# Performance work log

Measured on AMD Instinct MI355X. Metric: run time of the kernel, lower is better.

Reference implementation:

```python
import jax, jax.numpy as jnp
import numpy as np
from itertools import product

B, C, HH, WW, DD, N = 2, 32, 96, 96, 96, 30000


def setup_inputs() -> dict:
    key = jax.random.key(0)
    k1, k2, k3 = jax.random.split(key, 3)
    voxel_features = jax.random.normal(k1, (B, C, HH, WW, DD), dtype=jnp.float32)
    # vertices in normalized [-1, 1] grid_sample coordinates (x, y, z)
    vertices = jax.random.uniform(k2, (B, N, 3), dtype=jnp.float32, minval=-1.0, maxval=1.0)
    fan_in = C * 27
    conv_w = jax.random.normal(k3, (C, C, 1, 27), dtype=jnp.float32) * np.sqrt(2.0 / fan_in)
    conv_b = jnp.zeros((C,), dtype=jnp.float32)
    return {
        "voxel_features": voxel_features,
        "vertices": vertices,
        "conv_w": conv_w,
        "conv_b": conv_b,
        "img_H": HH,
        "img_W": WW,
        "img_D": DD,
    }


def _trilinear_sample(voxel_features, grid):
    """grid_sample(mode='bilinear', padding_mode='border', align_corners=True).
    voxel_features: (B,C,H,W,D); grid: (B,N,K,3) with (x,y,z) in [-1,1],
    x -> D axis, y -> W axis, z -> H axis. Returns (B,C,N,K)."""
    b, c, h, w, d = voxel_features.shape
    x, y, z = grid[..., 0], grid[..., 1], grid[..., 2]
    ix = jnp.clip((x + 1.0) * 0.5 * (d - 1), 0.0, d - 1)
    iy = jnp.clip((y + 1.0) * 0.5 * (w - 1), 0.0, w - 1)
    iz = jnp.clip((z + 1.0) * 0.5 * (h - 1), 0.0, h - 1)
    x0 = jnp.floor(ix).astype(jnp.int32); x1 = jnp.minimum(x0 + 1, d - 1)
    y0 = jnp.floor(iy).astype(jnp.int32); y1 = jnp.minimum(y0 + 1, w - 1)
    z0 = jnp.floor(iz).astype(jnp.int32); z1 = jnp.minimum(z0 + 1, h - 1)
    fx = ix - x0; fy = iy - y0; fz = iz - z0
    vf = voxel_features.reshape(b, c, h * w * d)
    n, k = grid.shape[1], grid.shape[2]

    def gather(zi, yi, xi):
        lin = (zi * w + yi) * d + xi  # (B,N,K)
        g = jnp.take_along_axis(vf, lin.reshape(b, 1, n * k), axis=2)
        return g.reshape(b, c, n, k)

    def wgt(wz, wy, wx):
        return (wz * wy * wx)[:, None]  # (B,1,N,K)

    out = (
        gather(z0, y0, x0) * wgt(1 - fz, 1 - fy, 1 - fx)
        + gather(z0, y0, x1) * wgt(1 - fz, 1 - fy, fx)
        + gather(z0, y1, x0) * wgt(1 - fz, fy, 1 - fx)
        + gather(z0, y1, x1) * wgt(1 - fz, fy, fx)
        + gather(z1, y0, x0) * wgt(fz, 1 - fy, 1 - fx)
        + gather(z1, y0, x1) * wgt(fz, 1 - fy, fx)
        + gather(z1, y1, x0) * wgt(fz, fy, 1 - fx)
        + gather(z1, y1, x1) * wgt(fz, fy, fx)
    )
    return out


def reference(voxel_features, vertices, conv_w, conv_b, img_H, img_W, img_D):
    # 27 neighbor offsets in normalized coords, scaled per (x,y,z) component
    offs = jnp.asarray(list(product((-1, 0, 1), repeat=3)), dtype=jnp.float32)  # (27,3)
    scale = jnp.array(
        [2.0 / (img_D - 1), 2.0 / (img_W - 1), 2.0 / (img_H - 1)], dtype=jnp.float32
    )
    shift = offs * scale  # (27,3)
    grid = vertices[:, :, None, :] + shift[None, None]  # (B,N,27,3)
    feats = _trilinear_sample(voxel_features, grid)  # (B,C,N,27)
    # Conv2d(C,C,(1,27)): weighted reduction over (C_in, 27) -> (B,N,C_out)
    out = jnp.einsum("bink,oik->bno", feats, conv_w[:, :, 0, :]) + conv_b
    return out
```

## Files before the change

kernel.cpp:

```cpp
#include <hip/hip_runtime.h>
#include <stdint.h>

#define HWD 884736ull
#define NV 30000
#define AST 1032

typedef __attribute__((ext_vector_type(8))) __bf16 bf16x8;
typedef __attribute__((ext_vector_type(4))) float f32x4;
typedef __attribute__((ext_vector_type(2))) float f32x2;
typedef __attribute__((ext_vector_type(4))) unsigned int uint4v;

__device__ __forceinline__ unsigned short f2bf(float f) {
    union { float f; unsigned int u; } v; v.f = f;
    unsigned int u = v.u;
    return (unsigned short)((u + 0x7FFFu + ((u >> 16) & 1u)) >> 16);
}

__device__ __forceinline__ unsigned short bfc(float f) {
    __bf16 h = (__bf16)f;
    unsigned short u;
    __builtin_memcpy(&u, &h, 2);
    return u;
}

__device__ __forceinline__ unsigned int pkbf(float lo, float hi) {
    __bf16 a = (__bf16)lo, b = (__bf16)hi;
    unsigned short ua, ub;
    __builtin_memcpy(&ua, &a, 2);
    __builtin_memcpy(&ub, &b, 2);
    return (unsigned int)ua | ((unsigned int)ub << 16);
}

__device__ __forceinline__ f32x2 up2(unsigned int u) {
    union { unsigned int u; float f; } lo, hi;
    lo.u = u << 16;
    hi.u = u & 0xFFFF0000u;
    f32x2 r; r.x = lo.f; r.y = hi.f;
    return r;
}

__device__ __forceinline__ void axis_setup(float coord, float sc, int& wstart, float w[3][4]) {
    int i0[3], i1[3];
    float fr[3];
#pragma unroll
    for (int a = 0; a < 3; ++a) {
        float g = coord + (float)(a - 1) * sc;
        float ix = (g + 1.0f) * 0.5f * 95.0f;
        ix = fminf(fmaxf(ix, 0.0f), 95.0f);
        float fl = floorf(ix);
        int x0 = (int)fl;
        i0[a] = x0;
        i1[a] = min(x0 + 1, 95);
        fr[a] = ix - fl;
    }
    int ws = min(max(i0[1] - 1, 0), 92);
    wstart = ws;
#pragma unroll
    for (int a = 0; a < 3; ++a) {
        int d0 = min(max(i0[a] - ws, 0), 3);
        int d1 = min(max(i1[a] - ws, 0), 3);
        float f1 = fr[a], f0 = 1.0f - f1;
#pragma unroll
        for (int j = 0; j < 4; ++j)
            w[a][j] = (d0 == j ? f0 : 0.0f) + (d1 == j ? f1 : 0.0f);
    }
}

__global__ __launch_bounds__(256) void prep_kernel(const float* __restrict__ cw,
                                                   unsigned short* __restrict__ Wp) {
    int gid = blockIdx.x * 256 + threadIdx.x;
    int j = gid & 7;
    int l = (gid >> 3) & 63;
    int t = (gid >> 9) & 1;
    int s = gid >> 10;
    int kk = ((l >> 4) & 3) * 8 + j;
    int o = t * 16 + (l & 15);
    float v = 0.0f;
    if (kk < 27) v = cw[(size_t)o * 864 + s * 27 + kk];
    Wp[gid] = f2bf(v);
}

__global__ __launch_bounds__(256) void transpose_kernel(const float* __restrict__ vox,
                                                        unsigned short* __restrict__ voxT) {
    __shared__ unsigned short T[192 * 40];
    int blk = blockIdx.x;
    int tid = threadIdx.x;
    int b = blk / 4608;
    int zy = blk - b * 4608;
    const float* src = vox + (size_t)b * 32 * HWD + (size_t)zy * 192;
    int c = tid >> 3;
    int xs = tid & 7;
    const float* srcc = src + (size_t)c * HWD;
#pragma unroll
    for (int i = 0; i < 6; ++i) {
        int x4 = xs + 8 * i;
        f32x4 v = *(const f32x4*)(srcc + x4 * 4);
#pragma unroll
        for (int k = 0; k < 4; ++k)
            T[(x4 * 4 + k) * 40 + c] = bfc(v[k]);
    }
    __syncthreads();
    unsigned short* dst = voxT + (size_t)blk * 6144;
#pragma unroll
    for (int i = 0; i < 3; ++i) {
        int q = i * 256 + tid;
        int x = q >> 2;
        int cg = (q & 3) * 8;
        uint4v val = *(const uint4v*)&T[x * 40 + cg];
        *(uint4v*)(dst + q * 8) = val;
    }
}

__global__ __launch_bounds__(256) void fused_kernel(const unsigned short* __restrict__ voxT,
                                                    const float* __restrict__ verts,
                                                    const unsigned short* __restrict__ Wp,
                                                    const float* __restrict__ bias,
                                                    float* __restrict__ out) {
    __shared__ unsigned short At[16 * AST];
    int tid = threadIdx.x;
    int vl = tid >> 4;
    int cp = tid & 15;
    int vg = (int)blockIdx.x * 16 + vl;

    const float* vp = verts + (size_t)vg * 3;
    float vx = vp[0], vy = vp[1], vz = vp[2];
    const float sc = 2.0f / 95.0f;
    int wsx, wsy, wsz;
    float wx[3][4], wy[3][4], wz[3][4];
    axis_setup(vx, sc, wsx, wx);
    axis_setup(vy, sc, wsy, wy);
    axis_setup(vz, sc, wsz, wz);
    int bb = (vg >= NV) ? 1 : 0;
    const unsigned short* vb = voxT + (size_t)bb * HWD * 32 + 2 * cp;

    f32x2 zz = {0.f, 0.f};
    f32x2 f[27];
#pragma unroll
    for (int k = 0; k < 27; ++k) f[k] = zz;

#pragma unroll
    for (int tz = 0; tz < 4; ++tz) {
        f32x2 ry[3][3];
#pragma unroll
        for (int bq = 0; bq < 3; ++bq)
#pragma unroll
            for (int a = 0; a < 3; ++a) ry[bq][a] = zz;
#pragma unroll
        for (int ty = 0; ty < 4; ++ty) {
            const unsigned short* row =
                vb + (((size_t)(wsz + tz) * 96 + (size_t)(wsy + ty)) * 96 + wsx) * 32;
            unsigned int u0 = *(const unsigned int*)(row);
            unsigned int u1 = *(const unsigned int*)(row + 32);
            unsigned int u2 = *(const unsigned int*)(row + 64);
            unsigned int u3 = *(const unsigned int*)(row + 96);
            f32x2 b0 = up2(u0), b1 = up2(u1), b2 = up2(u2), b3 = up2(u3);
#pragma unroll
            for (int a = 0; a < 3; ++a) {
                f32x2 r = b0 * wx[a][0] + b1 * wx[a][1] + b2 * wx[a][2] + b3 * wx[a][3];
#pragma unroll
                for (int bq = 0; bq < 3; ++bq)
                    ry[bq][a] += r * wy[bq][ty];
            }
        }
#pragma unroll
        for (int g = 0; g < 3; ++g)
#pragma unroll
            for (int bq = 0; bq < 3; ++bq)
#pragma unroll
                for (int a = 0; a < 3; ++a)
                    f[9 * a + 3 * bq + g] += wz[g][tz] * ry[bq][a];
    }

    unsigned int pk0[16], pk1[16];
#pragma unroll
    for (int i = 0; i < 16; ++i) {
        float l0 = (2 * i < 27) ? f[2 * i].x : 0.0f;
        float h0 = (2 * i + 1 < 27) ? f[2 * i + 1].x : 0.0f;
        float l1 = (2 * i < 27) ? f[2 * i].y : 0.0f;
        float h1 = (2 * i + 1 < 27) ? f[2 * i + 1].y : 0.0f;
        pk0[i] = pkbf(l0, h0);
        pk1[i] = pkbf(l1, h1);
    }
    unsigned short* abase = &At[vl * AST + cp * 64];
    int e = cp & 7;
    {
        uint4v c0 = {pk0[0], pk0[1], pk0[2], pk0[3]};
        uint4v c1 = {pk0[4], pk0[5], pk0[6], pk0[7]};
        uint4v c2 = {pk0[8], pk0[9], pk0[10], pk0[11]};
        uint4v c3 = {pk0[12], pk0[13], pk0[14], pk0[15]};
        uint4v c4 = {pk1[0], pk1[1], pk1[2], pk1[3]};
        uint4v c5 = {pk1[4], pk1[5], pk1[6], pk1[7]};
        uint4v c6 = {pk1[8], pk1[9], pk1[10], pk1[11]};
        uint4v c7 = {pk1[12], pk1[13], pk1[14], pk1[15]};
        *(uint4v*)(abase + ((0 ^ e) << 3)) = c0;
        *(uint4v*)(abase + ((1 ^ e) << 3)) = c1;
        *(uint4v*)(abase + ((2 ^ e) << 3)) = c2;
        *(uint4v*)(abase + ((3 ^ e) << 3)) = c3;
        *(uint4v*)(abase + ((4 ^ e) << 3)) = c4;
        *(uint4v*)(abase + ((5 ^ e) << 3)) = c5;
        *(uint4v*)(abase + ((6 ^ e) << 3)) = c6;
        *(uint4v*)(abase + ((7 ^ e) << 3)) = c7;
    }

    __syncthreads();

    int wv = tid >> 6;
    if (wv < 2) {
        int lane = tid & 63;
        int mrow = lane & 15, quad = lane >> 4;
        const bf16x8* wp = (const bf16x8*)Wp;
        f32x4 acc = {0.f, 0.f, 0.f, 0.f};
#pragma unroll 8
        for (int s = 0; s < 32; ++s) {
            int cpg = s >> 1;
            int kk = ((s & 1) << 2) | quad;
            bf16x8 a = *(const bf16x8*)&At[mrow * AST + cpg * 64 + ((kk ^ (cpg & 7)) << 3)];
            bf16x8 b = wp[(s * 2 + wv) * 64 + lane];
            acc = __builtin_amdgcn_mfma_f32_16x16x32_bf16(a, b, acc, 0, 0, 0);
        }
        float bs = bias[wv * 16 + mrow];
#pragma unroll
        for (int r = 0; r < 4; ++r) {
            int v = (int)blockIdx.x * 16 + quad * 4 + r;
            out[(size_t)v * 32 + wv * 16 + mrow] = acc[r] + bs;
        }
    }
}

extern "C" void kernel_launch(void* const* d_in, const int* in_sizes, int n_in,
                              void* d_out, int out_size, void* d_ws, size_t ws_size,
                              hipStream_t stream) {
    const float* vox = (const float*)d_in[0];
    const float* verts = (const float*)d_in[1];
    const float* cw = (const float*)d_in[2];
    const float* cb = (const float*)d_in[3];
    float* out = (float*)d_out;

    unsigned short* Wp = (unsigned short*)d_ws;
    unsigned short* voxT = (unsigned short*)((char*)d_ws + 65536);

    hipLaunchKernelGGL(prep_kernel, dim3(128), dim3(256), 0, stream, cw, Wp);
    hipLaunchKernelGGL(transpose_kernel, dim3(9216), dim3(256), 0, stream, vox, voxT);
    hipLaunchKernelGGL(fused_kernel, dim3(3750), dim3(256), 0, stream,
                       voxT, verts, Wp, cb, out);
}
```

Before: 386.0 us.

## Exploit sparse z-weights, emit bf16 features directly to LDS per z-group

The z-axis interpolation now uses only the two nonzero tap indices per output z-offset instead of looping over all four z rows with mostly-zero weights. Results for each z-group are written as individual bf16 halfwords straight into the swizzled LDS tile, and the padding slots are zeroed up front. This removes the 27-entry f32x2 accumulator array to cut register pressure, and adds a launch-bounds occupancy hint of 4. The cost is 6 z-row passes instead of 4, giving more (mostly L1/L2-cached) global loads, and many scalar 2-byte LDS stores replacing eight 16-byte stores.

After: 393.0 us. No clear change (+1.8%).

```diff
diff --git a/kernel.cpp b/kernel.cpp
--- a/kernel.cpp
+++ b/kernel.cpp
@@ -21,14 +21,6 @@
     unsigned short u;
     __builtin_memcpy(&u, &h, 2);
     return u;
-}
-
-__device__ __forceinline__ unsigned int pkbf(float lo, float hi) {
-    __bf16 a = (__bf16)lo, b = (__bf16)hi;
-    unsigned short ua, ub;
-    __builtin_memcpy(&ua, &a, 2);
-    __builtin_memcpy(&ub, &b, 2);
-    return (unsigned int)ua | ((unsigned int)ub << 16);
 }
 
 __device__ __forceinline__ f32x2 up2(unsigned int u) {
@@ -63,6 +55,32 @@
 #pragma unroll
         for (int j = 0; j < 4; ++j)
             w[a][j] = (d0 == j ? f0 : 0.0f) + (d1 == j ? f1 : 0.0f);
+    }
+}
+
+__device__ __forceinline__ void axis_setup_z(float coord, float sc, int& wstart,
+                                             int dz[3][2], float fzw[3][2]) {
+    int i0[3], i1[3];
+    float fr[3];
+#pragma unroll
+    for (int a = 0; a < 3; ++a) {
+        float g = coord + (float)(a - 1) * sc;
+        float ix = (g + 1.0f) * 0.5f * 95.0f;
+        ix = fminf(fmaxf(ix, 0.0f), 95.0f);
+        float fl = floorf(ix);
+        int x0 = (int)fl;
+        i0[a] = x0;
+        i1[a] = min(x0 + 1, 95);
+        fr[a] = ix - fl;
+    }
+    int ws = min(max(i0[1] - 1, 0), 92);
+    wstart = ws;
+#pragma unroll
+    for (int a = 0; a < 3; ++a) {
+        dz[a][0] = min(max(i0[a] - ws, 0), 3);
+        dz[a][1] = min(max(i1[a] - ws, 0), 3);
+        fzw[a][0] = 1.0f - fr[a];
+        fzw[a][1] = fr[a];
     }
 }
 
@@ -111,11 +129,11 @@
     }
 }
 
-__global__ __launch_bounds__(256) void fused_kernel(const unsigned short* __restrict__ voxT,
-                                                    const float* __restrict__ verts,
-                                                    const unsigned short* __restrict__ Wp,
-                                                    const float* __restrict__ bias,
-                                                    float* __restrict__ out) {
+__global__ __launch_bounds__(256, 4) void fused_kernel(const unsigned short* __restrict__ voxT,
+                                                       const float* __restrict__ verts,
+                                                       const unsigned short* __restrict__ Wp,
+                                                       const float* __restrict__ bias,
+                                                       float* __restrict__ out) {
     __shared__ unsigned short At[16 * AST];
     int tid = threadIdx.x;
     int vl = tid >> 4;
@@ -126,80 +144,75 @@
     float vx = vp[0], vy = vp[1], vz = vp[2];
     const float sc = 2.0f / 95.0f;
     int wsx, wsy, wsz;
-    float wx[3][4], wy[3][4], wz[3][4];
+    float wx[3][4], wy[3][4];
+    int dzt[3][2];
+    float fzw[3][2];
     axis_setup(vx, sc, wsx, wx);
     axis_setup(vy, sc, wsy, wy);
-    axis_setup(vz, sc, wsz, wz);
+    axis_setup_z(vz, sc, wsz, dzt, fzw);
     int bb = (vg >= NV) ? 1 : 0;
     const unsigned short* vb = voxT + (size_t)bb * HWD * 32 + 2 * cp;
 
+    int e = cp & 7;
+    unsigned short* lanebase = &At[vl * AST + cp * 64];
+    unsigned short* bptr[8];
+#pragma unroll
+    for (int kc = 0; kc < 8; ++kc) bptr[kc] = lanebase + ((kc ^ e) << 3);
+
+#pragma unroll
+    for (int chi = 0; chi < 2; ++chi) {
+        unsigned short* p = bptr[chi * 4 + 3];
+        p[3] = 0;
+        *(unsigned long long*)(p + 4) = 0ull;
+    }
+
     f32x2 zz = {0.f, 0.f};
-    f32x2 f[27];
-#pragma unroll
-    for (int k = 0; k < 27; ++k) f[k] = zz;
-
-#pragma unroll
-    for (int tz = 0; tz < 4; ++tz) {
-        f32x2 ry[3][3];
+#pragma unroll
+    for (int g = 0; g < 3; ++g) {
+        f32x2 fg[9];
+#pragma unroll
+        for (int i = 0; i < 9; ++i) fg[i] = zz;
+#pragma unroll
+        for (int t2 = 0; t2 < 2; ++t2) {
+            int tz = dzt[g][t2];
+            float wzv = fzw[g][t2];
+            f32x2 ry[3][3];
+#pragma unroll
+            for (int bq = 0; bq < 3; ++bq)
+#pragma unroll
+                for (int a = 0; a < 3; ++a) ry[bq][a] = zz;
+#pragma unroll
+            for (int ty = 0; ty < 4; ++ty) {
+                const unsigned short* row =
+                    vb + (((size_t)(wsz + tz) * 96 + (size_t)(wsy + ty)) * 96 + wsx) * 32;
+                unsigned int u0 = *(const unsigned int*)(row);
+                unsigned int u1 = *(const unsigned int*)(row + 32);
+                unsigned int u2 = *(const unsigned int*)(row + 64);
+                unsigned int u3 = *(const unsigned int*)(row + 96);
+                f32x2 b0 = up2(u0), b1 = up2(u1), b2 = up2(u2), b3 = up2(u3);
+#pragma unroll
+                for (int a = 0; a < 3; ++a) {
+                    f32x2 r = b0 * wx[a][0] + b1 * wx[a][1] + b2 * wx[a][2] + b3 * wx[a][3];
+#pragma unroll
+                    for (int bq = 0; bq < 3; ++bq)
+                        ry[bq][a] += r * wy[bq][ty];
+                }
+            }
+#pragma unroll
+            for (int bq = 0; bq < 3; ++bq)
+#pragma unroll
+                for (int a = 0; a < 3; ++a)
+                    fg[3 * bq + a] += wzv * ry[bq][a];
+        }
 #pragma unroll
         for (int bq = 0; bq < 3; ++bq)
 #pragma unroll
-            for (int a = 0; a < 3; ++a) ry[bq][a] = zz;
-#pragma unroll
-        for (int ty = 0; ty < 4; ++ty) {
-            const unsigned short* row =
-                vb + (((size_t)(wsz + tz) * 96 + (size_t)(wsy + ty)) * 96 + wsx) * 32;
-            unsigned int u0 = *(const unsigned int*)(row);
-            unsigned int u1 = *(const unsigned int*)(row + 32);
-            unsigned int u2 = *(const unsigned int*)(row + 64);
-            unsigned int u3 = *(const unsigned int*)(row + 96);
-            f32x2 b0 = up2(u0), b1 = up2(u1), b2 = up2(u2), b3 = up2(u3);
-#pragma unroll
             for (int a = 0; a < 3; ++a) {
-                f32x2 r = b0 * wx[a][0] + b1 * wx[a][1] + b2 * wx[a][2] + b3 * wx[a][3];
-#pragma unroll
-                for (int bq = 0; bq < 3; ++bq)
-                    ry[bq][a] += r * wy[bq][ty];
+                int k1 = 9 * a + 3 * bq + g;
+                f32x2 v = fg[3 * bq + a];
+                bptr[k1 >> 3][k1 & 7] = bfc(v.x);
+                bptr[4 + (k1 >> 3)][k1 & 7] = bfc(v.y);
             }
-        }
-#pragma unroll
-        for (int g = 0; g < 3; ++g)
-#pragma unroll
-            for (int bq = 0; bq < 3; ++bq)
-#pragma unroll
-                for (int a = 0; a < 3; ++a)
-                    f[9 * a + 3 * bq + g] += wz[g][tz] * ry[bq][a];
-    }
-
-    unsigned int pk0[16], pk1[16];
-#pragma unroll
-    for (int i = 0; i < 16; ++i) {
-        float l0 = (2 * i < 27) ? f[2 * i].x : 0.0f;
-        float h0 = (2 * i + 1 < 27) ? f[2 * i + 1].x : 0.0f;
-        float l1 = (2 * i < 27) ? f[2 * i].y : 0.0f;
-        float h1 = (2 * i + 1 < 27) ? f[2 * i + 1].y : 0.0f;
-        pk0[i] = pkbf(l0, h0);
-        pk1[i] = pkbf(l1, h1);
-    }
-    unsigned short* abase = &At[vl * AST + cp * 64];
-    int e = cp & 7;
-    {
-        uint4v c0 = {pk0[0], pk0[1], pk0[2], pk0[3]};
-        uint4v c1 = {pk0[4], pk0[5], pk0[6], pk0[7]};
-        uint4v c2 = {pk0[8], pk0[9], pk0[10], pk0[11]};
-        uint4v c3 = {pk0[12], pk0[13], pk0[14], pk0[15]};
-        uint4v c4 = {pk1[0], pk1[1], pk1[2], pk1[3]};
-        uint4v c5 = {pk1[4], pk1[5], pk1[6], pk1[7]};
-        uint4v c6 = {pk1[8], pk1[9], pk1[10], pk1[11]};
-        uint4v c7 = {pk1[12], pk1[13], pk1[14], pk1[15]};
-        *(uint4v*)(abase + ((0 ^ e) << 3)) = c0;
-        *(uint4v*)(abase + ((1 ^ e) << 3)) = c1;
-        *(uint4v*)(abase + ((2 ^ e) << 3)) = c2;
-        *(uint4v*)(abase + ((3 ^ e) << 3)) = c3;
-        *(uint4v*)(abase + ((4 ^ e) << 3)) = c4;
-        *(uint4v*)(abase + ((5 ^ e) << 3)) = c5;
-        *(uint4v*)(abase + ((6 ^ e) << 3)) = c6;
-        *(uint4v*)(abase + ((7 ^ e) << 3)) = c7;
     }
 
     __syncthreads();
```

## Bin vertices spatially and remap blocks per XCD for gather locality

Applied to the files above, without the earlier changes.

Adds a counting-sort pipeline (zero, count, scan, scatter) that groups vertices into 8^3-voxel spatial bins per batch, producing a permutation. The fused kernel processes vertices in permuted order and remaps block indices so consecutive bins land on the same XCD, aiming to raise L2 hit rates for the random trilinear gathers. It adds four small kernel launches and an indirect write of outputs, and the scatter order is nondeterministic within a bin.

Result: slower. 414.6 us (+7.4%).

```diff
diff --git a/kernel.cpp b/kernel.cpp
--- a/kernel.cpp
+++ b/kernel.cpp
@@ -4,6 +4,7 @@
 #define HWD 884736ull
 #define NV 30000
 #define AST 1032
+#define NBIN 4096
 
 typedef __attribute__((ext_vector_type(8))) __bf16 bf16x8;
 typedef __attribute__((ext_vector_type(4))) float f32x4;
@@ -21,14 +22,6 @@
     unsigned short u;
     __builtin_memcpy(&u, &h, 2);
     return u;
-}
-
-__device__ __forceinline__ unsigned int pkbf(float lo, float hi) {
-    __bf16 a = (__bf16)lo, b = (__bf16)hi;
-    unsigned short ua, ub;
-    __builtin_memcpy(&ua, &a, 2);
-    __builtin_memcpy(&ub, &b, 2);
-    return (unsigned int)ua | ((unsigned int)ub << 16);
 }
 
 __device__ __forceinline__ f32x2 up2(unsigned int u) {
@@ -63,6 +56,63 @@
 #pragma unroll
         for (int j = 0; j < 4; ++j)
             w[a][j] = (d0 == j ? f0 : 0.0f) + (d1 == j ? f1 : 0.0f);
+    }
+}
+
+__device__ __forceinline__ int bin_of(const float* __restrict__ verts, int v) {
+    float x = verts[(size_t)v * 3 + 0];
+    float y = verts[(size_t)v * 3 + 1];
+    float z = verts[(size_t)v * 3 + 2];
+    float ix = fminf(fmaxf((x + 1.0f) * 0.5f * 95.0f, 0.0f), 95.0f);
+    float iy = fminf(fmaxf((y + 1.0f) * 0.5f * 95.0f, 0.0f), 95.0f);
+    float iz = fminf(fmaxf((z + 1.0f) * 0.5f * 95.0f, 0.0f), 95.0f);
+    int cx = ((int)ix) >> 3;
+    int cy = ((int)iy) >> 3;
+    int cz = ((int)iz) >> 3;
+    int b = (v >= NV) ? 1 : 0;
+    return ((b * 12 + cz) * 12 + cy) * 12 + cx;
+}
+
+__global__ __launch_bounds__(256) void zero_bins_kernel(unsigned int* __restrict__ cur) {
+    cur[blockIdx.x * 256 + threadIdx.x] = 0u;
+}
+
+__global__ __launch_bounds__(256) void bin_count_kernel(const float* __restrict__ verts,
+                                                        unsigned int* __restrict__ cur) {
+    int v = blockIdx.x * 256 + threadIdx.x;
+    if (v < 2 * NV) atomicAdd(&cur[bin_of(verts, v)], 1u);
+}
+
+__global__ __launch_bounds__(256) void scan_kernel(unsigned int* __restrict__ cur) {
+    __shared__ unsigned int s[NBIN];
+    __shared__ unsigned int w[256];
+    int tid = threadIdx.x;
+#pragma unroll
+    for (int i = 0; i < 16; ++i) s[i * 256 + tid] = cur[i * 256 + tid];
+    __syncthreads();
+    unsigned int loc[16];
+    unsigned int sum = 0;
+#pragma unroll
+    for (int i = 0; i < 16; ++i) { loc[i] = sum; sum += s[tid * 16 + i]; }
+    w[tid] = sum;
+    __syncthreads();
+    if (tid == 0) {
+        unsigned int a = 0;
+        for (int j = 0; j < 256; ++j) { unsigned int t = w[j]; w[j] = a; a += t; }
+    }
+    __syncthreads();
+    unsigned int base = w[tid];
+#pragma unroll
+    for (int i = 0; i < 16; ++i) cur[tid * 16 + i] = base + loc[i];
+}
+
+__global__ __launch_bounds__(256) void scatter_kernel(const float* __restrict__ verts,
+                                                      unsigned int* __restrict__ cur,
+                                                      int* __restrict__ perm) {
+    int v = blockIdx.x * 256 + threadIdx.x;
+    if (v < 2 * NV) {
+        unsigned int pos = atomicAdd(&cur[bin_of(verts, v)], 1u);
+        perm[pos] = v;
     }
 }
 
@@ -113,14 +163,22 @@
 
 __global__ __launch_bounds__(256) void fused_kernel(const unsigned short* __restrict__ voxT,
                                                     const float* __restrict__ verts,
+                                                    const int* __restrict__ perm,
                                                     const unsigned short* __restrict__ Wp,
                                                     const float* __restrict__ bias,
                                                     float* __restrict__ out) {
     __shared__ unsigned short At[16 * AST];
+    __shared__ int sh_ids[16];
+    int pb = (int)blockIdx.x;
+    int xcd = pb & 7;
+    int idx = pb >> 3;
+    int lblk = (xcd < 6) ? xcd * 469 + idx : 6 * 469 + (xcd - 6) * 468 + idx;
+
     int tid = threadIdx.x;
     int vl = tid >> 4;
     int cp = tid & 15;
-    int vg = (int)blockIdx.x * 16 + vl;
+    int vg = perm[lblk * 16 + vl];
+    if (cp == 0) sh_ids[vl] = vg;
 
     const float* vp = verts + (size_t)vg * 3;
     float vx = vp[0], vy = vp[1], vz = vp[2];
@@ -178,8 +236,8 @@
         float h0 = (2 * i + 1 < 27) ? f[2 * i + 1].x : 0.0f;
         float l1 = (2 * i < 27) ? f[2 * i].y : 0.0f;
         float h1 = (2 * i + 1 < 27) ? f[2 * i + 1].y : 0.0f;
-        pk0[i] = pkbf(l0, h0);
-        pk1[i] = pkbf(l1, h1);
+        pk0[i] = (unsigned int)bfc(l0) | ((unsigned int)bfc(h0) << 16);
+        pk1[i] = (unsigned int)bfc(l1) | ((unsigned int)bfc(h1) << 16);
     }
     unsigned short* abase = &At[vl * AST + cp * 64];
     int e = cp & 7;
@@ -221,7 +279,7 @@
         float bs = bias[wv * 16 + mrow];
 #pragma unroll
         for (int r = 0; r < 4; ++r) {
-            int v = (int)blockIdx.x * 16 + quad * 4 + r;
+            int v = sh_ids[quad * 4 + r];
             out[(size_t)v * 32 + wv * 16 + mrow] = acc[r] + bs;
         }
     }
@@ -238,9 +296,16 @@
 
     unsigned short* Wp = (unsigned short*)d_ws;
     unsigned short* voxT = (unsigned short*)((char*)d_ws + 65536);
-
+    char* tail = (char*)d_ws + 65536 + 2ull * HWD * 32 * 2;
+    unsigned int* cur = (unsigned int*)tail;
+    int* perm = (int*)(tail + NBIN * 4);
+
+    hipLaunchKernelGGL(zero_bins_kernel, dim3(16), dim3(256), 0, stream, cur);
+    hipLaunchKernelGGL(bin_count_kernel, dim3(235), dim3(256), 0, stream, verts, cur);
+    hipLaunchKernelGGL(scan_kernel, dim3(1), dim3(256), 0, stream, cur);
+    hipLaunchKernelGGL(scatter_kernel, dim3(235), dim3(256), 0, stream, verts, cur, perm);
     hipLaunchKernelGGL(prep_kernel, dim3(128), dim3(256), 0, stream, cw, Wp);
     hipLaunchKernelGGL(transpose_kernel, dim3(9216), dim3(256), 0, stream, vox, voxT);
     hipLaunchKernelGGL(fused_kernel, dim3(3750), dim3(256), 0, stream,
-                       voxT, verts, Wp, cb, out);
-}
+                       voxT, verts, perm, Wp, cb, out);
+}
```
